# Optimization experiments

Measured on AMD Instinct MI355X. Metric: run time of the kernel, lower is better.

The kernel has to match this reference:

```python
import jax, jax.numpy as jnp
import numpy as np

N = 1 << 20
SCALE = 20.0
NUM_EXPERTS = 39
MAX_LOG = 20.0
RESOLUTION = 0.125


def setup_inputs() -> dict:
    key = jax.random.key(0)
    k1, k2, k3 = jax.random.split(key, 3)
    a = jax.random.normal(k1, (N,), dtype=jnp.float32) * 100.0
    b = jax.random.normal(k2, (N,), dtype=jnp.float32) * 10.0
    opcode = jax.random.randint(k3, (N,), 0, NUM_EXPERTS).astype(jnp.int32)
    # LogDivision buffers: keys at 0.125 resolution, values 2^-k (161 entries)
    num_entries = int(MAX_LOG / RESOLUTION) + 1
    log_keys = jnp.arange(num_entries, dtype=jnp.float32) * RESOLUTION
    recip_values = jnp.power(jnp.float32(2.0), -log_keys).astype(jnp.float32)
    return {"a": a, "b": b, "log_keys": log_keys,
            "recip_values": recip_values, "opcode": opcode}


def _sharp_gate(x):
    # (silu(x*s + 0.5*s) - silu(x*s - 0.5*s)) / s  ~= step function
    return (jax.nn.silu(x * SCALE + 0.5 * SCALE)
            - jax.nn.silu(x * SCALE - 0.5 * SCALE)) / SCALE


def _eq_gate(d):
    # eq_gate(a,b) with d = a - b
    return _sharp_gate(d + 0.5) * _sharp_gate(0.5 - d)


def reference(a, b, log_keys, recip_values, opcode):
    op_f = opcode.astype(jnp.float32)
    expert_ids = jnp.arange(NUM_EXPERTS, dtype=jnp.float32)
    # OpcodeRouter: 39-way eq-gate, one-hot at matching opcode  [N, 39]
    gates = _eq_gate(op_f[:, None] - expert_ids[None, :])

    # LogDivision: a/b = a * 2^(-log2(b)) via softmax attention over table
    b_pos = b > 0
    log_b = jnp.log2(jnp.abs(jnp.where(b_pos, b, jnp.float32(1.0))))
    scores = -jnp.abs(log_keys[None, :] - log_b[:, None]) * 50.0  # [N, 161]
    w = jax.nn.softmax(scores, axis=-1)
    recip = w @ recip_values  # [N]
    div = jnp.where(b_pos, jnp.floor(a * recip), jnp.float32(0.0))
    # mod: 0 if b==0 else a - div*b (div is 0 for b<=0, as in torch source)
    mod = jnp.where(b == 0, jnp.float32(0.0), a - div * b)

    # BitwiseExpert (integer casts, zero-gradient paths)
    ai = a.astype(jnp.int32)
    bi = b.astype(jnp.int32)
    shamt = jnp.clip(bi, 0, 31)  # guard undefined shifts
    or_ = (ai | bi).astype(jnp.float32)
    xor_ = (ai ^ bi).astype(jnp.float32)
    and_ = (ai & bi).astype(jnp.float32)
    shl = (ai << shamt).astype(jnp.float32)
    shr = (ai >> shamt).astype(jnp.float32)

    # ComparisonExpert via sharp gates
    d = a - b
    eq = _eq_gate(d)
    ne = 1.0 - eq
    lt = _sharp_gate(b - a - 0.5)
    gt = _sharp_gate(a - b - 0.5)
    le = _sharp_gate(b - a + 0.5)
    ge = _sharp_gate(a - b + 0.5)

    # Expert results for opcodes 14..29: OR,XOR,AND,EQ,NE,LT,GT,LE,GE,SHL,SHR,ADD,SUB,MUL,DIV,MOD
    results = jnp.stack([or_, xor_, and_, eq, ne, lt, gt, le, ge,
                         shl, shr, a + b, a - b, a * b, div, mod], axis=-1)
    out = jnp.einsum('ne,ne->n', gates[:, 14:30], results)
    return out
```

## Files before the change

kernel.cpp:

```cpp
#include <hip/hip_runtime.h>


static constexpr int BLOCK = 256;

__device__ __forceinline__ float siluf(float x) {
    return x / (1.0f + __expf(-x));
}
__device__ __forceinline__ float sharp_gatef(float x) {
    float t = x * 20.0f;
    return (siluf(t + 10.0f) - siluf(t - 10.0f)) * 0.05f;
}
__device__ __forceinline__ float eq_gatef(float d) {
    return sharp_gatef(d + 0.5f) * sharp_gatef(0.5f - d);
}

__device__ __forceinline__ float compute_one(float a, float b, int op,
                                             const float* __restrict__ recip_tbl) {
    float out = 0.0f;
    if (op >= 14 && op <= 29) {
        if (op <= 16 || op == 23 || op == 24) {
            int ai = (int)a, bi = (int)b;
            int r;
            switch (op) {
                case 14: r = ai | bi; break;
                case 15: r = ai ^ bi; break;
                case 16: r = ai & bi; break;
                case 23: { int sh = bi < 0 ? 0 : (bi > 31 ? 31 : bi);
                           r = (int)(((unsigned)ai) << sh); } break;
                default: { int sh = bi < 0 ? 0 : (bi > 31 ? 31 : bi);
                           r = ai >> sh; } break;
            }
            out = (float)r;
        } else if (op >= 17 && op <= 22) {
            float d = a - b;
            switch (op) {
                case 17: out = eq_gatef(d); break;
                case 18: out = 1.0f - eq_gatef(d); break;
                case 19: out = sharp_gatef(-d - 0.5f); break;
                case 20: out = sharp_gatef(d - 0.5f);  break;
                case 21: out = sharp_gatef(-d + 0.5f); break;
                default: out = sharp_gatef(d + 0.5f);  break;
            }
        } else if (op == 25) { out = a + b; }
        else if (op == 26) { out = a - b; }
        else if (op == 27) { out = a * b; }
        else {
            float dv = 0.0f;
            if (b > 0.0f) {
                float logb = __log2f(b);
                int i0 = (int)floorf(logb * 8.0f + 0.5f);
                i0 = i0 < 0 ? 0 : (i0 > 160 ? 160 : i0);
                int lo = i0 - 3 < 0 ? 0 : i0 - 3;
                int hi = i0 + 3 > 160 ? 160 : i0 + 3;
                float dmin = fabsf((float)i0 * 0.125f - logb);
                float wsum = 0.0f, rsum = 0.0f;
                for (int k = lo; k <= hi; ++k) {
                    float dk = fabsf((float)k * 0.125f - logb);
                    float w = __expf(-50.0f * (dk - dmin));
                    wsum += w;
                    rsum += w * recip_tbl[k];
                }
                dv = floorf(a * (rsum / wsum));
            }
            if (op == 28) out = dv;
            else out = (b == 0.0f) ? 0.0f : (a - dv * b);
        }
    }
    return out;
}

__global__ __launch_bounds__(BLOCK) void c4_kernel(
        const float* __restrict__ A, const float* __restrict__ B,
        const int* __restrict__ OP, const float* __restrict__ recip_tbl,
        float* __restrict__ OUT, int n4, int n) {
    int i = blockIdx.x * BLOCK + threadIdx.x;
    if (i < n4) {
        float4 a4 = reinterpret_cast<const float4*>(A)[i];
        float4 b4 = reinterpret_cast<const float4*>(B)[i];
        int4   o4 = reinterpret_cast<const int4*>(OP)[i];
        float4 r;
        r.x = compute_one(a4.x, b4.x, o4.x, recip_tbl);
        r.y = compute_one(a4.y, b4.y, o4.y, recip_tbl);
        r.z = compute_one(a4.z, b4.z, o4.z, recip_tbl);
        r.w = compute_one(a4.w, b4.w, o4.w, recip_tbl);
        reinterpret_cast<float4*>(OUT)[i] = r;
    }
    if (i == 0) {
        for (int j = n4 * 4; j < n; ++j)
            OUT[j] = compute_one(A[j], B[j], OP[j], recip_tbl);
    }
}

extern "C" void kernel_launch(void* const* d_in, const int* in_sizes, int n_in,
                              void* d_out, int out_size, void* d_ws, size_t ws_size,
                              hipStream_t stream) {
    const float* A     = (const float*)d_in[0];
    const float* B     = (const float*)d_in[1];
    const float* recip = (const float*)d_in[3];
    const int*   OP    = (const int*)d_in[4];
    float* OUT = (float*)d_out;
    int n  = in_sizes[0];
    int n4 = n / 4;
    int blocks = (n4 + BLOCK - 1) / BLOCK;
    if (blocks < 1) blocks = 1;
    c4_kernel<<<blocks, BLOCK, 0, stream>>>(A, B, OP, recip, OUT, n4, n);
}
```

Measured before the change: 80.37 us.

## Compute all expert results branch-free with shared-exp gates and select by opcode

```diff
diff --git a/kernel.cpp b/kernel.cpp
--- a/kernel.cpp
+++ b/kernel.cpp
@@ -3,70 +3,69 @@
 
 static constexpr int BLOCK = 256;
 
-__device__ __forceinline__ float siluf(float x) {
-    return x / (1.0f + __expf(-x));
-}
-__device__ __forceinline__ float sharp_gatef(float x) {
-    float t = x * 20.0f;
-    return (siluf(t + 10.0f) - siluf(t - 10.0f)) * 0.05f;
-}
-__device__ __forceinline__ float eq_gatef(float d) {
-    return sharp_gatef(d + 0.5f) * sharp_gatef(0.5f - d);
-}
-
 __device__ __forceinline__ float compute_one(float a, float b, int op,
                                              const float* __restrict__ recip_tbl) {
-    float out = 0.0f;
-    if (op >= 14 && op <= 29) {
-        if (op <= 16 || op == 23 || op == 24) {
-            int ai = (int)a, bi = (int)b;
-            int r;
-            switch (op) {
-                case 14: r = ai | bi; break;
-                case 15: r = ai ^ bi; break;
-                case 16: r = ai & bi; break;
-                case 23: { int sh = bi < 0 ? 0 : (bi > 31 ? 31 : bi);
-                           r = (int)(((unsigned)ai) << sh); } break;
-                default: { int sh = bi < 0 ? 0 : (bi > 31 ? 31 : bi);
-                           r = ai >> sh; } break;
-            }
-            out = (float)r;
-        } else if (op >= 17 && op <= 22) {
-            float d = a - b;
-            switch (op) {
-                case 17: out = eq_gatef(d); break;
-                case 18: out = 1.0f - eq_gatef(d); break;
-                case 19: out = sharp_gatef(-d - 0.5f); break;
-                case 20: out = sharp_gatef(d - 0.5f);  break;
-                case 21: out = sharp_gatef(-d + 0.5f); break;
-                default: out = sharp_gatef(d + 0.5f);  break;
-            }
-        } else if (op == 25) { out = a + b; }
-        else if (op == 26) { out = a - b; }
-        else if (op == 27) { out = a * b; }
-        else {
-            float dv = 0.0f;
-            if (b > 0.0f) {
-                float logb = __log2f(b);
-                int i0 = (int)floorf(logb * 8.0f + 0.5f);
-                i0 = i0 < 0 ? 0 : (i0 > 160 ? 160 : i0);
-                int lo = i0 - 3 < 0 ? 0 : i0 - 3;
-                int hi = i0 + 3 > 160 ? 160 : i0 + 3;
-                float dmin = fabsf((float)i0 * 0.125f - logb);
-                float wsum = 0.0f, rsum = 0.0f;
-                for (int k = lo; k <= hi; ++k) {
-                    float dk = fabsf((float)k * 0.125f - logb);
-                    float w = __expf(-50.0f * (dk - dmin));
-                    wsum += w;
-                    rsum += w * recip_tbl[k];
-                }
-                dv = floorf(a * (rsum / wsum));
-            }
-            if (op == 28) out = dv;
-            else out = (b == 0.0f) ? 0.0f : (a - dv * b);
-        }
+    int ai = (int)a, bi = (int)b;
+    int sh = bi < 0 ? 0 : (bi > 31 ? 31 : bi);
+    float fOr  = (float)(ai | bi);
+    float fXor = (float)(ai ^ bi);
+    float fAnd = (float)(ai & bi);
+    float fShl = (float)((int)(((unsigned)ai) << sh));
+    float fShr = (float)(ai >> sh);
+
+    const float EM20 = 2.0611536e-9f;
+    const float EP20 = 4.8516520e+8f;
+    float d = a - b;
+    float t = 20.0f * d;
+    float E = __expf(-t);
+    float sp = (t + 20.0f) / (1.0f + E * EM20);
+    float s0 = t          / (1.0f + E);
+    float sm = (t - 20.0f) / (1.0f + E * EP20);
+    float ge = (sp - s0) * 0.05f;
+    float gt = (s0 - sm) * 0.05f;
+    float lt = 1.0f - ge;
+    float le = 1.0f - gt;
+    float eq = ge * le;
+    float ne = 1.0f - eq;
+
+    float logb = __log2f(b);
+    float fi0 = floorf(logb * 8.0f + 0.5f);
+    fi0 = fminf(fmaxf(fi0, 0.0f), 160.0f);
+    int i0 = (int)fi0;
+    i0 = i0 < 0 ? 0 : (i0 > 160 ? 160 : i0);
+    float d0 = fabsf((float)i0 * 0.125f - logb);
+    float wsum = 0.0f, rsum = 0.0f;
+#pragma unroll
+    for (int j = -1; j <= 1; ++j) {
+        int k = i0 + j;
+        k = k < 0 ? 0 : (k > 160 ? 160 : k);
+        float dk = fabsf((float)k * 0.125f - logb);
+        float w = __expf(-50.0f * (dk - d0));
+        wsum += w;
+        rsum += w * recip_tbl[k];
     }
-    return out;
+    float dvraw = floorf(a * (rsum / wsum));
+    float dv  = (b > 0.0f) ? dvraw : 0.0f;
+    float mod = (b == 0.0f) ? 0.0f : (a - dv * b);
+
+    float r =
+        op == 14 ? fOr  :
+        op == 15 ? fXor :
+        op == 16 ? fAnd :
+        op == 17 ? eq   :
+        op == 18 ? ne   :
+        op == 19 ? lt   :
+        op == 20 ? gt   :
+        op == 21 ? le   :
+        op == 22 ? ge   :
+        op == 23 ? fShl :
+        op == 24 ? fShr :
+        op == 25 ? a + b :
+        op == 26 ? a - b :
+        op == 27 ? a * b :
+        op == 28 ? dv   :
+        op == 29 ? mod  : 0.0f;
+    return r;
 }
 
 __global__ __launch_bounds__(BLOCK) void c4_kernel(
```

After: 72.94 us. 1.1x faster.
